# Optimization experiments

Measured on AMD Instinct MI355X. Metric: run time of the kernel, lower is better.

The kernel has to match this reference:

```python
import jax, jax.numpy as jnp
import numpy as np

N, D, K, M = 1024, 128, 256, 4
H, NB = 256, 2  # QINCoStep defaults: hidden_dim=256, num_res_blocks=2


def setup_inputs() -> dict:
    key = jax.random.key(0)
    ks = jax.random.split(key, 6)
    z = jax.random.normal(ks[0], (N, D), jnp.float32)
    base_cb = jax.random.normal(ks[1], (M, K, D), jnp.float32) * 0.1
    cp_w = jax.random.normal(ks[2], (M, D, 2 * D), jnp.float32) * (1.0 / np.sqrt(2 * D)).astype(np.float32)
    cp_b = jnp.zeros((M, D), jnp.float32)
    w1 = jax.random.normal(ks[3], (M, NB, H, D), jnp.float32) * (1.0 / np.sqrt(D)).astype(np.float32)
    b1 = jnp.zeros((M, NB, H), jnp.float32)
    w2 = jax.random.normal(ks[4], (M, NB, D, H), jnp.float32) * (1.0 / np.sqrt(H)).astype(np.float32)
    b2 = jnp.zeros((M, NB, D), jnp.float32)
    return dict(z=z, base_cb=base_cb, cp_w=cp_w, cp_b=cp_b, w1=w1, b1=b1, w2=w2, b2=b2)


def _encode_step(z, x_hat, cb, cpw, cpb, w1, b1, w2, b2):
    # concat_proj(Linear(2D,D)) on cat([x_hat, cbar]) decomposed into two GEMMs
    Wx, Wc = cpw[:, :D], cpw[:, D:]          # (D,D), (D,D)
    A = x_hat @ Wx.T                          # (N,D)
    B = cb @ Wc.T                             # (K,D)
    C = A[:, None, :] + B[None, :, :] + cpb   # (N,K,D) data-dependent codebook
    for i in range(NB):                       # residual MLP blocks
        h = jax.nn.relu(jnp.einsum('nkd,hd->nkh', C, w1[i]) + b1[i])
        C = C + jnp.einsum('nkh,dh->nkd', h, w2[i]) + b2[i]
    r = z - x_hat                             # (N,D) residual before step
    dists = jnp.sum((r[:, None, :] - C) ** 2, axis=-1)   # (N,K)
    codes = jnp.argmin(dists, axis=-1)        # (N,)
    c_sel = jnp.take_along_axis(C, codes[:, None, None], axis=1)[:, 0]  # (N,D)
    return codes, x_hat + c_sel, r, c_sel


def reference(z, base_cb, cp_w, cp_b, w1, b1, w2, b2):
    x_hat = jnp.zeros_like(z)
    codes_all, residuals, centroids = [], [], []
    for m in range(M):
        codes, x_hat, r, c_sel = _encode_step(
            z, x_hat, base_cb[m], cp_w[m], cp_b[m], w1[m], b1[m], w2[m], b2[m])
        codes_all.append(codes)
        residuals.append(r)
        centroids.append(c_sel)
    codes_all = jnp.stack(codes_all, axis=-1)          # (N,M)
    z_q = x_hat
    z_q_st = z + jax.lax.stop_gradient(z_q - z)        # straight-through
    return z_q_st, codes_all, jnp.stack(residuals), jnp.stack(centroids)
```

## Files before the change

kernel.cpp:

```cpp
#include <hip/hip_runtime.h>

#define N_ 1024
#define D_ 128
#define K_ 256
#define M_ 4
#define H_ 256
#define NB_ 2
#define KT_ 32
#define NTILE_ 8
#define EPS_ 0.12f
#define CHPAD 136
#define HPAD  264

typedef _Float16 half8 __attribute__((ext_vector_type(8)));
typedef __attribute__((ext_vector_type(8))) short short8;
typedef __attribute__((ext_vector_type(4))) float f32x4;
typedef __attribute__((ext_vector_type(16))) float f32x16;

__device__ inline float s2f(unsigned short s) {
    return (float)__builtin_bit_cast(_Float16, s);
}
__device__ inline unsigned short f2h(float x) {
    return __builtin_bit_cast(unsigned short, (_Float16)x);
}
__device__ inline void split2h(float x, unsigned short& hi, unsigned short& lo) {
    _Float16 h = (_Float16)x;
    _Float16 l = (_Float16)(x - (float)h);
    hi = __builtin_bit_cast(unsigned short, h);
    lo = __builtin_bit_cast(unsigned short, l);
}
__device__ inline f32x16 zero16() {
    f32x16 v;
    #pragma unroll
    for (int i = 0; i < 16; ++i) v[i] = 0.0f;
    return v;
}
__device__ inline void lds_barrier() {
    asm volatile("s_waitcnt lgkmcnt(0)" ::: "memory");
    __builtin_amdgcn_sched_barrier(0);
    __builtin_amdgcn_s_barrier();
    __builtin_amdgcn_sched_barrier(0);
}

__global__ void precompute_Bb(const float* __restrict__ base_cb,
                              const float* __restrict__ cp_w,
                              float* __restrict__ Bb) {
    const int mk = blockIdx.x;
    const int m  = mk >> 8;
    const int d  = threadIdx.x;
    const float* cb = base_cb + (size_t)mk * D_;
    const float* wc = cp_w + ((size_t)(m * D_ + d)) * (2 * D_) + D_;
    double a0 = 0, a1 = 0, a2 = 0, a3 = 0;
    #pragma unroll
    for (int dp = 0; dp < D_; dp += 4) {
        a0 += (double)(cb[dp + 0] * wc[dp + 0]);
        a1 += (double)(cb[dp + 1] * wc[dp + 1]);
        a2 += (double)(cb[dp + 2] * wc[dp + 2]);
        a3 += (double)(cb[dp + 3] * wc[dp + 3]);
    }
    Bb[(size_t)mk * D_ + d] = (float)((a0 + a1) + (a2 + a3));
}

__global__ void convert_w(const float* __restrict__ w1,
                          const float* __restrict__ w2,
                          unsigned short* __restrict__ w1pk,
                          unsigned short* __restrict__ w2pk) {
    const int i = blockIdx.x * blockDim.x + threadIdx.x;
    {
        const int e    = i & 7;
        const int sel  = (i >> 3) & 1;
        const int j32  = (i >> 4) & 31;
        const int kt   = (i >> 9) & 7;
        const int jblk = (i >> 12) & 7;
        const int bi   = i >> 15;
        const int j = jblk * 32 + j32;
        const int d = kt * 16 + sel * 8 + e;
        w1pk[i] = f2h(w1[((size_t)(bi * H_ + j)) * D_ + d]);
    }
    {
        const int e    = i & 7;
        const int sel  = (i >> 3) & 1;
        const int d32  = (i >> 4) & 31;
        const int s    = (i >> 9) & 15;
        const int dblk = (i >> 13) & 3;
        const int bi   = i >> 15;
        const int d = dblk * 32 + d32;
        const int hc = s * 16 + sel * 8 + e;
        w2pk[i] = f2h(w2[((size_t)(bi * D_ + d)) * H_ + hc]);
    }
}

__launch_bounds__(256, 4)
__global__ void mega_kernel(const float* __restrict__ z,
                            const float* __restrict__ cp_w,
                            const float* __restrict__ cp_b,
                            const float* __restrict__ w1,
                            const float* __restrict__ b1,
                            const float* __restrict__ w2,
                            const float* __restrict__ b2,
                            const float* __restrict__ Bb,
                            const unsigned short* __restrict__ w1pk,
                            const unsigned short* __restrict__ w2pk,
                            float* __restrict__ out0,
                            float* __restrict__ out1,
                            float* __restrict__ out2,
                            float* __restrict__ out3) {
    __shared__ alignas(16) unsigned short sChi[KT_][CHPAD];
    __shared__ alignas(16) unsigned short sClo[KT_][CHPAD];
    __shared__ alignas(16) unsigned short sHh[KT_][HPAD];
    __shared__ alignas(16) float sA[D_], sxhat[D_], sr[D_], scb[D_];
    __shared__ alignas(16) float sdist[K_];
    __shared__ float sE[D_], scsel[D_];
    __shared__ float shrow[H_];
    __shared__ double sdd[2];
    __shared__ float smin, sbest;
    __shared__ int   sbidx, supd;

    const int n    = blockIdx.x;
    const int t    = threadIdx.x;
    const int wid  = t >> 6;
    const int lane = t & 63;
    const int l31  = lane & 31;
    const int hi   = lane >> 5;
    const int koff = hi * 8;
    const int loff = (l31 * 2 + hi) * 8;

    if (t < D_) { sxhat[t] = 0.0f; sA[t] = 0.0f; }
    __syncthreads();

    for (int m = 0; m < M_; ++m) {
        if (t < D_) {
            scb[t] = cp_b[m * D_ + t];
            const float rv = z[(size_t)n * D_ + t] - sxhat[t];
            sr[t] = rv;
            out2[((size_t)m * N_ + n) * D_ + t] = rv;
        }
        lds_barrier();

        for (int tile = 0; tile < NTILE_; ++tile) {
            const int k0 = tile * KT_;

            {
                const int row  = t >> 3;
                const int dblk = (t & 7) * 16;
                const f32x4* bb4 = (const f32x4*)(Bb + ((size_t)(m * K_ + k0 + row)) * D_ + dblk);
                #pragma unroll
                for (int g = 0; g < 2; ++g) {
                    const f32x4 v0 = bb4[g * 2];
                    const f32x4 v1 = bb4[g * 2 + 1];
                    short8 hs, ls;
                    #pragma unroll
                    for (int x = 0; x < 8; ++x) {
                        const int d = dblk + g * 8 + x;
                        const float bv = (x < 4) ? v0[x] : v1[x - 4];
                        unsigned short ch, cl;
                        split2h((sA[d] + bv) + scb[d], ch, cl);
                        hs[x] = (short)ch;
                        ls[x] = (short)cl;
                    }
                    *(short8*)&sChi[row][dblk + g * 8] = hs;
                    *(short8*)&sClo[row][dblk + g * 8] = ls;
                }
            }
            lds_barrier();

            for (int i = 0; i < NB_; ++i) {
                const int bi = m * NB_ + i;

                half8 g2w[16];
                {
                    const int j0 = wid * 32 + l31;
                    const unsigned short* pA = w1pk + ((size_t)((bi * 8 + wid) * 8)) * 512 + loff;
                    const unsigned short* pB = w1pk + ((size_t)((bi * 8 + wid + 4) * 8)) * 512 + loff;
                    half8 wA[8], wB[8];
                    #pragma unroll
                    for (int kt = 0; kt < 8; ++kt) {
                        wA[kt] = *(const half8*)(pA + kt * 512);
                        wB[kt] = *(const half8*)(pB + kt * 512);
                    }
                    f32x16 aA = zero16(), aB = zero16();
                    #pragma unroll
                    for (int kt = 0; kt < 8; ++kt) {
                        half8 ah = *(const half8*)&sChi[l31][kt * 16 + koff];
                        half8 al = *(const half8*)&sClo[l31][kt * 16 + koff];
                        aA = __builtin_amdgcn_mfma_f32_32x32x16_f16(ah, wA[kt], aA, 0, 0, 0);
                        aB = __builtin_amdgcn_mfma_f32_32x32x16_f16(ah, wB[kt], aB, 0, 0, 0);
                        aA = __builtin_amdgcn_mfma_f32_32x32x16_f16(al, wA[kt], aA, 0, 0, 0);
                        aB = __builtin_amdgcn_mfma_f32_32x32x16_f16(al, wB[kt], aB, 0, 0, 0);
                    }
                    {
                        const unsigned short* pd =
                            w2pk + ((size_t)((bi * 4 + wid) * 16)) * 512 + loff;
                        #pragma unroll
                        for (int s = 0; s < 16; ++s)
                            g2w[s] = *(const half8*)(pd + s * 512);
                    }
                    const float b1A = b1[(size_t)bi * H_ + j0];
                    const float b1B = b1[(size_t)bi * H_ + j0 + 128];
                    #pragma unroll
                    for (int reg = 0; reg < 16; ++reg) {
                        const int krow = (reg & 3) + 8 * (reg >> 2) + 4 * hi;
                        sHh[krow][j0]       = f2h(fmaxf(aA[reg] + b1A, 0.0f));
                        sHh[krow][j0 + 128] = f2h(fmaxf(aB[reg] + b1B, 0.0f));
                    }
                }
                lds_barrier();

                {
                    const int d = wid * 32 + l31;
                    f32x16 c0a = zero16(), c0b = zero16();
                    #pragma unroll
                    for (int s = 0; s < 16; s += 2) {
                        half8 h0e = *(const half8*)&sHh[l31][s * 16 + koff];
                        half8 h0o = *(const half8*)&sHh[l31][(s + 1) * 16 + koff];
                        c0a = __builtin_amdgcn_mfma_f32_32x32x16_f16(h0e, g2w[s], c0a, 0, 0, 0);
                        c0b = __builtin_amdgcn_mfma_f32_32x32x16_f16(h0o, g2w[s + 1], c0b, 0, 0, 0);
                    }
                    const float b2v = b2[(size_t)bi * D_ + d];
                    #pragma unroll
                    for (int reg = 0; reg < 16; ++reg) {
                        const int krow = (reg & 3) + 8 * (reg >> 2) + 4 * hi;
                        const float cvo = s2f(sChi[krow][d]) + s2f(sClo[krow][d]);
                        const float cv  = (cvo + (c0a[reg] + c0b[reg])) + b2v;
                        unsigned short ch, cl;
                        split2h(cv, ch, cl);
                        sChi[krow][d] = ch;
                        sClo[krow][d] = cl;
                    }
                }
                lds_barrier();
            }

            if (t < 128) {
                const int row = t >> 2, seg = t & 3;
                float qa = 0.f;
                #pragma unroll
                for (int dd = 0; dd < 32; ++dd) {
                    const int d = seg * 32 + dd;
                    const float cv = s2f(sChi[row][d]) + s2f(sClo[row][d]);
                    const float e = sr[d] - cv;
                    qa = fmaf(e, e, qa);
                }
                qa += __shfl_xor(qa, 1);
                qa += __shfl_xor(qa, 2);
                if (seg == 0) sdist[k0 + row] = qa;
            }
            lds_barrier();
        }

        if (t < 64) {
            float bv = fminf(fminf(sdist[t], sdist[t + 64]),
                             fminf(sdist[t + 128], sdist[t + 192]));
            #pragma unroll
            for (int s = 1; s < 64; s <<= 1) bv = fminf(bv, __shfl_xor(bv, s));
            if (t == 0) { smin = bv; sbest = 1e30f; sbidx = 0; }
        }
        __syncthreads();
        const float thr = smin + EPS_;

        for (int k = 0; k < K_; ++k) {
            if (sdist[k] > thr) continue;
            if (t < D_)
                sE[t] = (sA[t] + Bb[((size_t)(m * K_ + k)) * D_ + t]) + scb[t];
            __syncthreads();
            for (int i = 0; i < NB_; ++i) {
                const int bi = m * NB_ + i;
                {
                    const f32x4* wp = (const f32x4*)(w1 + ((size_t)bi * H_ + t) * D_);
                    double h0 = 0, h1 = 0, h2 = 0, h3 = 0;
                    #pragma unroll 8
                    for (int u = 0; u < 32; ++u) {
                        f32x4 wv = wp[u];
                        h0 += (double)(sE[u * 4 + 0] * wv[0]);
                        h1 += (double)(sE[u * 4 + 1] * wv[1]);
                        h2 += (double)(sE[u * 4 + 2] * wv[2]);
                        h3 += (double)(sE[u * 4 + 3] * wv[3]);
                    }
                    const float hv = (float)((h0 + h1) + (h2 + h3)) + b1[(size_t)bi * H_ + t];
                    shrow[t] = fmaxf(hv, 0.0f);
                }
                __syncthreads();
                if (t < D_) {
                    const f32x4* wp = (const f32x4*)(w2 + ((size_t)bi * D_ + t) * H_);
                    double s0 = 0, s1 = 0, s2 = 0, s3 = 0;
                    #pragma unroll 8
                    for (int u = 0; u < 64; ++u) {
                        f32x4 wv = wp[u];
                        s0 += (double)(shrow[u * 4 + 0] * wv[0]);
                        s1 += (double)(shrow[u * 4 + 1] * wv[1]);
                        s2 += (double)(shrow[u * 4 + 2] * wv[2]);
                        s3 += (double)(shrow[u * 4 + 3] * wv[3]);
                    }
                    sE[t] = (sE[t] + (float)((s0 + s1) + (s2 + s3))) + b2[(size_t)bi * D_ + t];
                }
                __syncthreads();
            }
            {
                double dp = 0.0;
                if (t < D_) {
                    const float e = sr[t] - sE[t];
                    const float e2 = e * e;
                    dp = (double)e2;
                    #pragma unroll
                    for (int s = 1; s < 64; s <<= 1) dp += __shfl_xor(dp, s);
                    if ((t & 63) == 0) sdd[t >> 6] = dp;
                }
            }
            __syncthreads();
            if (t == 0) {
                const float df = (float)(sdd[0] + sdd[1]);
                if (df < sbest) { sbest = df; sbidx = k; supd = 1; }
                else supd = 0;
            }
            __syncthreads();
            if (supd && t < D_) scsel[t] = sE[t];
            __syncthreads();
        }

        if (t == 0) out1[(size_t)n * M_ + m] = (float)sbidx;

        if (t < D_) {
            const float cs = scsel[t];
            out3[((size_t)m * N_ + n) * D_ + t] = cs;
            const float xnew = sxhat[t] + cs;
            sxhat[t] = xnew;
            if (m == M_ - 1) {
                const float zv = z[(size_t)n * D_ + t];
                out0[(size_t)n * D_ + t] = zv + (xnew - zv);
            }
        }
        __syncthreads();

        if (m < M_ - 1 && t < D_) {
            const f32x4* wp = (const f32x4*)(cp_w + ((size_t)((m + 1) * D_ + t)) * (2 * D_));
            double a0 = 0, a1 = 0, a2 = 0, a3 = 0;
            #pragma unroll 8
            for (int u = 0; u < 32; ++u) {
                f32x4 wv = wp[u];
                a0 += (double)(sxhat[u * 4 + 0] * wv[0]);
                a1 += (double)(sxhat[u * 4 + 1] * wv[1]);
                a2 += (double)(sxhat[u * 4 + 2] * wv[2]);
                a3 += (double)(sxhat[u * 4 + 3] * wv[3]);
            }
            sA[t] = (float)((a0 + a1) + (a2 + a3));
        }
        __syncthreads();
    }
}

extern "C" void kernel_launch(void* const* d_in, const int* in_sizes, int n_in,
                              void* d_out, int out_size, void* d_ws, size_t ws_size,
                              hipStream_t stream) {
    const float* z       = (const float*)d_in[0];
    const float* base_cb = (const float*)d_in[1];
    const float* cp_w    = (const float*)d_in[2];
    const float* cp_b    = (const float*)d_in[3];
    const float* w1      = (const float*)d_in[4];
    const float* b1      = (const float*)d_in[5];
    const float* w2      = (const float*)d_in[6];
    const float* b2      = (const float*)d_in[7];

    float* out  = (float*)d_out;
    float* out0 = out;
    float* out1 = out0 + (size_t)N_ * D_;
    float* out2 = out1 + (size_t)N_ * M_;
    float* out3 = out2 + (size_t)M_ * N_ * D_;

    char* ws = (char*)d_ws;
    float*          Bb   = (float*)(ws + 0);
    unsigned short* w1pk = (unsigned short*)(ws + 524288);
    unsigned short* w2pk = (unsigned short*)(ws + 1048576);

    hipLaunchKernelGGL(precompute_Bb, dim3(M_ * K_), dim3(D_), 0, stream,
                       base_cb, cp_w, Bb);
    hipLaunchKernelGGL(convert_w, dim3(1024), dim3(256), 0, stream,
                       w1, w2, w1pk, w2pk);
    hipLaunchKernelGGL(mega_kernel, dim3(N_), dim3(256), 0, stream,
                       z, cp_w, cp_b, w1, b1, w2, b2, Bb,
                       w1pk, w2pk,
                       out0, out1, out2, out3);
}
```

Baseline: 878.2 us.

## Skip exact recheck when one candidate is within margin; store final C as fp32

```diff
diff --git a/kernel.cpp b/kernel.cpp
--- a/kernel.cpp
+++ b/kernel.cpp
@@ -8,8 +8,9 @@
 #define NB_ 2
 #define KT_ 32
 #define NTILE_ 8
-#define EPS_ 0.12f
+#define EPS_ 0.08f
 #define CHPAD 136
+#define CFS 132
 #define HPAD  264
 
 typedef _Float16 half8 __attribute__((ext_vector_type(8)));
@@ -105,16 +106,20 @@
                             float* __restrict__ out1,
                             float* __restrict__ out2,
                             float* __restrict__ out3) {
-    __shared__ alignas(16) unsigned short sChi[KT_][CHPAD];
-    __shared__ alignas(16) unsigned short sClo[KT_][CHPAD];
+    __shared__ alignas(16) unsigned short sCbuf[2 * KT_ * CHPAD];
     __shared__ alignas(16) unsigned short sHh[KT_][HPAD];
     __shared__ alignas(16) float sA[D_], sxhat[D_], sr[D_], scb[D_];
     __shared__ alignas(16) float sdist[K_];
     __shared__ float sE[D_], scsel[D_];
     __shared__ float shrow[H_];
     __shared__ double sdd[2];
-    __shared__ float smin, sbest;
+    __shared__ float smin;
+    __shared__ float sbest;
     __shared__ int   sbidx, supd;
+
+    #define CHI(r, c) (sCbuf[(r) * CHPAD + (c)])
+    #define CLO(r, c) (sCbuf[KT_ * CHPAD + (r) * CHPAD + (c)])
+    #define CFC(r, c) (((float*)sCbuf)[(r) * CFS + (c)])
 
     const int n    = blockIdx.x;
     const int t    = threadIdx.x;
@@ -124,6 +129,7 @@
     const int hi   = lane >> 5;
     const int koff = hi * 8;
     const int loff = (l31 * 2 + hi) * 8;
+    const int dcol = wid * 32 + l31;
 
     if (t < D_) { sxhat[t] = 0.0f; sA[t] = 0.0f; }
     __syncthreads();
@@ -158,14 +164,15 @@
                         hs[x] = (short)ch;
                         ls[x] = (short)cl;
                     }
-                    *(short8*)&sChi[row][dblk + g * 8] = hs;
-                    *(short8*)&sClo[row][dblk + g * 8] = ls;
+                    *(short8*)&CHI(row, dblk + g * 8) = hs;
+                    *(short8*)&CLO(row, dblk + g * 8) = ls;
                 }
             }
             lds_barrier();
 
             for (int i = 0; i < NB_; ++i) {
                 const int bi = m * NB_ + i;
+                f32x16 cvo = zero16();
 
                 half8 g2w[16];
                 {
@@ -181,8 +188,8 @@
                     f32x16 aA = zero16(), aB = zero16();
                     #pragma unroll
                     for (int kt = 0; kt < 8; ++kt) {
-                        half8 ah = *(const half8*)&sChi[l31][kt * 16 + koff];
-                        half8 al = *(const half8*)&sClo[l31][kt * 16 + koff];
+                        half8 ah = *(const half8*)&CHI(l31, kt * 16 + koff);
+                        half8 al = *(const half8*)&CLO(l31, kt * 16 + koff);
                         aA = __builtin_amdgcn_mfma_f32_32x32x16_f16(ah, wA[kt], aA, 0, 0, 0);
                         aB = __builtin_amdgcn_mfma_f32_32x32x16_f16(ah, wB[kt], aB, 0, 0, 0);
                         aA = __builtin_amdgcn_mfma_f32_32x32x16_f16(al, wA[kt], aA, 0, 0, 0);
@@ -203,12 +210,19 @@
                         sHh[krow][j0]       = f2h(fmaxf(aA[reg] + b1A, 0.0f));
                         sHh[krow][j0 + 128] = f2h(fmaxf(aB[reg] + b1B, 0.0f));
                     }
+                    if (i == NB_ - 1) {
+                        #pragma unroll
+                        for (int reg = 0; reg < 16; ++reg) {
+                            const int krow = (reg & 3) + 8 * (reg >> 2) + 4 * hi;
+                            cvo[reg] = s2f(CHI(krow, dcol)) + s2f(CLO(krow, dcol));
+                        }
+                    }
                 }
                 lds_barrier();
 
                 {
-                    const int d = wid * 32 + l31;
-                    f32x16 c0a = zero16(), c0b = zero16();
+                    f32x16 c0a = (i == NB_ - 1) ? cvo : zero16();
+                    f32x16 c0b = zero16();
                     #pragma unroll
                     for (int s = 0; s < 16; s += 2) {
                         half8 h0e = *(const half8*)&sHh[l31][s * 16 + koff];
@@ -216,33 +230,45 @@
                         c0a = __builtin_amdgcn_mfma_f32_32x32x16_f16(h0e, g2w[s], c0a, 0, 0, 0);
                         c0b = __builtin_amdgcn_mfma_f32_32x32x16_f16(h0o, g2w[s + 1], c0b, 0, 0, 0);
                     }
-                    const float b2v = b2[(size_t)bi * D_ + d];
-                    #pragma unroll
-                    for (int reg = 0; reg < 16; ++reg) {
-                        const int krow = (reg & 3) + 8 * (reg >> 2) + 4 * hi;
-                        const float cvo = s2f(sChi[krow][d]) + s2f(sClo[krow][d]);
-                        const float cv  = (cvo + (c0a[reg] + c0b[reg])) + b2v;
-                        unsigned short ch, cl;
-                        split2h(cv, ch, cl);
-                        sChi[krow][d] = ch;
-                        sClo[krow][d] = cl;
+                    const float b2v = b2[(size_t)bi * D_ + dcol];
+                    if (i < NB_ - 1) {
+                        #pragma unroll
+                        for (int reg = 0; reg < 16; ++reg) {
+                            const int krow = (reg & 3) + 8 * (reg >> 2) + 4 * hi;
+                            const float cvr = s2f(CHI(krow, dcol)) + s2f(CLO(krow, dcol));
+                            const float cv  = (cvr + (c0a[reg] + c0b[reg])) + b2v;
+                            unsigned short ch, cl;
+                            split2h(cv, ch, cl);
+                            CHI(krow, dcol) = ch;
+                            CLO(krow, dcol) = cl;
+                        }
+                    } else {
+                        #pragma unroll
+                        for (int reg = 0; reg < 16; ++reg) {
+                            const int krow = (reg & 3) + 8 * (reg >> 2) + 4 * hi;
+                            CFC(krow, dcol) = (c0a[reg] + c0b[reg]) + b2v;
+                        }
                     }
                 }
                 lds_barrier();
             }
 
-            if (t < 128) {
-                const int row = t >> 2, seg = t & 3;
+            {
+                const int row = t >> 3, seg = t & 7, db = seg * 16;
                 float qa = 0.f;
                 #pragma unroll
-                for (int dd = 0; dd < 32; ++dd) {
-                    const int d = seg * 32 + dd;
-                    const float cv = s2f(sChi[row][d]) + s2f(sClo[row][d]);
-                    const float e = sr[d] - cv;
-                    qa = fmaf(e, e, qa);
+                for (int g = 0; g < 4; ++g) {
+                    const f32x4 cv = *(const f32x4*)&CFC(row, db + g * 4);
+                    const f32x4 rv = *(const f32x4*)&sr[db + g * 4];
+                    #pragma unroll
+                    for (int x = 0; x < 4; ++x) {
+                        const float e = rv[x] - cv[x];
+                        qa = fmaf(e, e, qa);
+                    }
                 }
                 qa += __shfl_xor(qa, 1);
                 qa += __shfl_xor(qa, 2);
+                qa += __shfl_xor(qa, 4);
                 if (seg == 0) sdist[k0 + row] = qa;
             }
             lds_barrier();
@@ -257,9 +283,13 @@
         }
         __syncthreads();
         const float thr = smin + EPS_;
-
-        for (int k = 0; k < K_; ++k) {
-            if (sdist[k] > thr) continue;
+        const int flag = (sdist[t] <= thr) ? 1 : 0;
+        const int cnt = __syncthreads_count(flag);
+
+        if (cnt == 1) {
+            if (flag) sbidx = t;
+            __syncthreads();
+            const int k = sbidx;
             if (t < D_)
                 sE[t] = (sA[t] + Bb[((size_t)(m * K_ + k)) * D_ + t]) + scb[t];
             __syncthreads();
@@ -295,26 +325,67 @@
                 }
                 __syncthreads();
             }
-            {
-                double dp = 0.0;
-                if (t < D_) {
-                    const float e = sr[t] - sE[t];
-                    const float e2 = e * e;
-                    dp = (double)e2;
-                    #pragma unroll
-                    for (int s = 1; s < 64; s <<= 1) dp += __shfl_xor(dp, s);
-                    if ((t & 63) == 0) sdd[t >> 6] = dp;
-                }
-            }
+            if (t < D_) scsel[t] = sE[t];
             __syncthreads();
-            if (t == 0) {
-                const float df = (float)(sdd[0] + sdd[1]);
-                if (df < sbest) { sbest = df; sbidx = k; supd = 1; }
-                else supd = 0;
-            }
-            __syncthreads();
-            if (supd && t < D_) scsel[t] = sE[t];
-            __syncthreads();
+        } else {
+            for (int k = 0; k < K_; ++k) {
+                if (sdist[k] > thr) continue;
+                if (t < D_)
+                    sE[t] = (sA[t] + Bb[((size_t)(m * K_ + k)) * D_ + t]) + scb[t];
+                __syncthreads();
+                for (int i = 0; i < NB_; ++i) {
+                    const int bi = m * NB_ + i;
+                    {
+                        const f32x4* wp = (const f32x4*)(w1 + ((size_t)bi * H_ + t) * D_);
+                        double h0 = 0, h1 = 0, h2 = 0, h3 = 0;
+                        #pragma unroll 8
+                        for (int u = 0; u < 32; ++u) {
+                            f32x4 wv = wp[u];
+                            h0 += (double)(sE[u * 4 + 0] * wv[0]);
+                            h1 += (double)(sE[u * 4 + 1] * wv[1]);
+                            h2 += (double)(sE[u * 4 + 2] * wv[2]);
+                            h3 += (double)(sE[u * 4 + 3] * wv[3]);
+                        }
+                        const float hv = (float)((h0 + h1) + (h2 + h3)) + b1[(size_t)bi * H_ + t];
+                        shrow[t] = fmaxf(hv, 0.0f);
+                    }
+                    __syncthreads();
+                    if (t < D_) {
+                        const f32x4* wp = (const f32x4*)(w2 + ((size_t)bi * D_ + t) * H_);
+                        double s0 = 0, s1 = 0, s2 = 0, s3 = 0;
+                        #pragma unroll 8
+                        for (int u = 0; u < 64; ++u) {
+                            f32x4 wv = wp[u];
+                            s0 += (double)(shrow[u * 4 + 0] * wv[0]);
+                            s1 += (double)(shrow[u * 4 + 1] * wv[1]);
+                            s2 += (double)(shrow[u * 4 + 2] * wv[2]);
+                            s3 += (double)(shrow[u * 4 + 3] * wv[3]);
+                        }
+                        sE[t] = (sE[t] + (float)((s0 + s1) + (s2 + s3))) + b2[(size_t)bi * D_ + t];
+                    }
+                    __syncthreads();
+                }
+                {
+                    double dp = 0.0;
+                    if (t < D_) {
+                        const float e = sr[t] - sE[t];
+                        const float e2 = e * e;
+                        dp = (double)e2;
+                        #pragma unroll
+                        for (int s = 1; s < 64; s <<= 1) dp += __shfl_xor(dp, s);
+                        if ((t & 63) == 0) sdd[t >> 6] = dp;
+                    }
+                }
+                __syncthreads();
+                if (t == 0) {
+                    const float df = (float)(sdd[0] + sdd[1]);
+                    if (df < sbest) { sbest = df; sbidx = k; supd = 1; }
+                    else supd = 0;
+                }
+                __syncthreads();
+                if (supd && t < D_) scsel[t] = sE[t];
+                __syncthreads();
+            }
         }
 
         if (t == 0) out1[(size_t)n * M_ + m] = (float)sbidx;
@@ -346,6 +417,9 @@
         }
         __syncthreads();
     }
+    #undef CHI
+    #undef CLO
+    #undef CFC
 }
 
 extern "C" void kernel_launch(void* const* d_in, const int* in_sizes, int n_in,
```

Measured after the change: 851.4 us, median of 2. 1.03x faster.
